# Performance work log

Hardware: AMD Instinct MI355X
Metric: run time of the kernel (lower is better)

The kernel has to match this reference:

```python
import jax, jax.numpy as jnp
import numpy as np

B, C, H, W = 2, 256, 48, 48
NH = 4          # heads (and SE ratio)
DK = C // NH    # 64


def conv1x1(x, w, b):
    # x: [B,Cin,H,W], w: [Cout,Cin], b: [Cout]
    return jnp.einsum('oc,bchw->bohw', w, x) + b[None, :, None, None]


def rtrans(q_in, k_in, v_in, qw, qb, kw, kb, vw, vb):
    b, c, h_, w_ = q_in.shape
    n = h_ * w_
    q = conv1x1(q_in, qw, qb).reshape(b, NH, DK, n).transpose(0, 1, 3, 2)  # [B,h,N,dk]
    k = conv1x1(k_in, kw, kb).reshape(b, NH, DK, n)                         # [B,h,dk,N]
    v = conv1x1(v_in, vw, vb).reshape(b, NH, DK, n)                         # [B,h,dk,N]
    scores = jnp.einsum('bhnd,bhdm->bhnm', q, k) / jnp.sqrt(jnp.asarray(DK, q.dtype))
    attn = jax.nn.softmax(scores, axis=-1)                                  # [B,h,N,N]
    out = jnp.einsum('bhdn,bhnm->bhdm', v, attn)                            # [B,h,dk,N]
    return out.reshape(b, c, h_, w_)


def setup_inputs() -> dict:
    key = jax.random.key(0)
    ks = jax.random.split(key, 16)
    s = 0.02
    d = {
        'x': jax.random.normal(ks[0], (B, C, H, W), jnp.float32),
        'y': jax.random.normal(ks[1], (B, C, H, W), jnp.float32),
        # RScaling: fc1 Conv2d(2C, C//ratio, 1), fc2 Conv2d(C//ratio, 2C, 1); ratio=NH
        'sc_fc1_w': jax.random.normal(ks[2], (C // NH, 2 * C), jnp.float32) * s,
        'sc_fc1_b': jnp.zeros((C // NH,), jnp.float32),
        'sc_fc2_w': jax.random.normal(ks[3], (2 * C, C // NH), jnp.float32) * s,
        'sc_fc2_b': jnp.zeros((2 * C,), jnp.float32),
        # RTrans 1
        't1_qw': jax.random.normal(ks[4], (C, C), jnp.float32) * s,
        't1_qb': jnp.zeros((C,), jnp.float32),
        't1_kw': jax.random.normal(ks[5], (C, C), jnp.float32) * s,
        't1_kb': jnp.zeros((C,), jnp.float32),
        't1_vw': jax.random.normal(ks[6], (C, C), jnp.float32) * s,
        't1_vb': jnp.zeros((C,), jnp.float32),
        # RTrans 2 (ST=True)
        't2_qw': jax.random.normal(ks[7], (C, C), jnp.float32) * s,
        't2_qb': jnp.zeros((C,), jnp.float32),
        't2_kw': jax.random.normal(ks[8], (C, C), jnp.float32) * s,
        't2_kb': jnp.zeros((C,), jnp.float32),
        't2_vw': jax.random.normal(ks[9], (C, C), jnp.float32) * s,
        't2_vb': jnp.zeros((C,), jnp.float32),
        # RGating: Conv2d(2C, 2, 1)
        'gate_w': jax.random.normal(ks[10], (2, 2 * C), jnp.float32) * s,
        'gate_b': jnp.zeros((2,), jnp.float32),
    }
    return d


def reference(x, y, sc_fc1_w, sc_fc1_b, sc_fc2_w, sc_fc2_b,
              t1_qw, t1_qb, t1_kw, t1_kb, t1_vw, t1_vb,
              t2_qw, t2_qb, t2_kw, t2_kb, t2_vw, t2_vb,
              gate_w, gate_b):
    c = x.shape[1]
    # --- RScaling (SE squeeze-excite on concatenated streams) ---
    cat = jnp.concatenate([x, y], axis=1)                       # [B,2C,H,W]
    pooled = cat.mean(axis=(2, 3), keepdims=True)               # [B,2C,1,1]
    f = conv1x1(jax.nn.relu(conv1x1(pooled, sc_fc1_w, sc_fc1_b)), sc_fc2_w, sc_fc2_b)
    g = jax.nn.sigmoid(f)                                       # [B,2C,1,1]
    x = x * g[:, :c] + x
    y = y * g[:, c:] + y
    # --- RTrans 1: x = attn(q=x, k=y, v=y) ---
    x = rtrans(x, y, y, t1_qw, t1_qb, t1_kw, t1_kb, t1_vw, t1_vb)
    # --- RTrans 2 (ST): y = attn(q=y, k=x_new, v=x_new) ---
    y = rtrans(y, x, x, t2_qw, t2_qb, t2_kw, t2_kb, t2_vw, t2_vb)
    # --- RGating ---
    gate = jax.nn.sigmoid(conv1x1(jnp.concatenate([x, y], axis=1), gate_w, gate_b))  # [B,2,H,W]
    x = x * gate[:, :1] + x
    y = y * gate[:, 1:] + y
    return (x, y)
```

## Files before the change

### kernel.cpp

```cpp
#include <hip/hip_runtime.h>
#include <hip/hip_bf16.h>
#include <math.h>

typedef __hip_bfloat16 bf16;
typedef unsigned short u16;
typedef __attribute__((ext_vector_type(8))) short short8;
typedef __attribute__((ext_vector_type(4))) float f32x4;

#define BB  2
#define CC  256
#define NHH 4
#define DKK 64
#define NN  2304
#define NT  36
#define NT2 18
#define MS  4
#define NTM 9
#define MFMA16(a,b,c) __builtin_amdgcn_mfma_f32_16x16x32_bf16(a, b, c, 0, 0, 0)

__device__ __forceinline__ float u2f(u16 u){ return __uint_as_float(((unsigned)u) << 16); }
__device__ __forceinline__ u16 f2u(float f){
    unsigned u = __float_as_uint(f);
    unsigned r = u + 0x7FFFu + ((u >> 16) & 1u);
    return (u16)(r >> 16);
}

__device__ __forceinline__ float ldv(const void* p, size_t i, int bf){
    return bf ? u2f(((const u16*)p)[i]) : ((const float*)p)[i];
}
__device__ __forceinline__ void stv(void* p, size_t i, float v, int bf){
    if (bf) ((u16*)p)[i] = f2u(v);
    else    ((float*)p)[i] = v;
}
__device__ __forceinline__ short8 ldw8(const void* p, size_t i, int bf){
    if (bf) return *(const short8*)((const u16*)p + i);
    const float* f = (const float*)p + i;
    short8 r;
    #pragma unroll
    for (int k = 0; k < 8; k++) r[k] = (short)f2u(f[k]);
    return r;
}

__global__ void detect_kernel(const void* __restrict__ x, int* __restrict__ flg){
    const u16* u = (const u16*)x;
    int t = threadIdx.x;
    bool ok = true;
    for (int i = 0; i < 8; i++){
        u16 v = u[t*8 + i];
        int e = (v >> 7) & 0xFF;
        ok = ok && (((v & 0x7FFF) == 0) || (e >= 96 && e <= 143));
    }
    unsigned long long b = __ballot(ok);
    if (t == 0) *flg = (b == 0xFFFFFFFFFFFFFFFFull) ? 1 : 0;
}

__global__ void pool_kernel(const void* __restrict__ x, const void* __restrict__ y,
                            const int* __restrict__ flg, float* __restrict__ pooled){
    int bf = *flg;
    int bid = blockIdx.x;
    int b = bid >> 9, cc = bid & 511;
    const void* src = (cc < CC) ? x : y;
    size_t base = ((size_t)b*CC + (cc & 255))*NN;
    float s = 0.f;
    for (int i = threadIdx.x; i < NN; i += 256) s += ldv(src, base + i, bf);
    __shared__ float red[4];
    for (int off = 32; off; off >>= 1) s += __shfl_down(s, off, 64);
    if ((threadIdx.x & 63) == 0) red[threadIdx.x >> 6] = s;
    __syncthreads();
    if (threadIdx.x == 0)
        pooled[bid] = (red[0]+red[1]+red[2]+red[3]) * (1.0f/(float)NN);
}

__global__ void se_fc1_kernel(const float* __restrict__ pooled,
                              const void* __restrict__ w1, const void* __restrict__ b1,
                              const int* __restrict__ flg, float* __restrict__ f1){
    int bf = *flg;
    int bid = blockIdx.x;
    int b = bid >> 6, f = bid & 63;
    int lane = threadIdx.x;
    const float* ps = pooled + b*512;
    float a = 0.f;
    #pragma unroll
    for (int k = 0; k < 8; k++){
        int c = lane*8 + k;
        a += ldv(w1, (size_t)f*512 + c, bf) * ps[c];
    }
    #pragma unroll
    for (int off = 32; off; off >>= 1) a += __shfl_down(a, off, 64);
    if (lane == 0)
        f1[b*64 + f] = fmaxf(a + ldv(b1, f, bf), 0.f);
}

__global__ void se_fc2_kernel(const float* __restrict__ f1,
                              const void* __restrict__ w2, const void* __restrict__ b2v,
                              const int* __restrict__ flg, float* __restrict__ gse){
    int bf = *flg;
    int b = blockIdx.x;
    int o = threadIdx.x;
    __shared__ float f1s[64];
    if (o < 64) f1s[o] = f1[b*64 + o];
    __syncthreads();
    float a = ldv(b2v, o, bf);
    #pragma unroll
    for (int j = 0; j < 64; j++) a += ldv(w2, (size_t)o*64 + j, bf) * f1s[j];
    gse[b*512 + o] = 1.f + 1.f/(1.f + __expf(-a));
}

__global__ void transpose2_kernel(const void* __restrict__ x, const void* __restrict__ y,
                                  const float* __restrict__ gse, const int* __restrict__ flg,
                                  u16* __restrict__ xsT, u16* __restrict__ ysT){
    int bf = *flg;
    int z = blockIdx.z;
    int b = z >> 1, which = z & 1;
    const void* src = which ? y : x;
    const float* gs = gse + b*512 + (which ? 256 : 0);
    u16* dst = which ? ysT : xsT;
    int ct = blockIdx.y, nt = blockIdx.x;
    int t = threadIdx.x;
    int nl = t & 63, cq = t >> 6;
    #pragma unroll
    for (int i = 0; i < 16; i++){
        int c = ct*64 + cq*16 + i;
        float v = ldv(src, ((size_t)b*CC + c)*NN + nt*64 + nl, bf) * gs[c];
        dst[((size_t)b*NN + nt*64 + nl)*CC + c] = f2u(v);
    }
}

__launch_bounds__(256)
__global__ void conv3_mfma(const u16* __restrict__ Xq, const u16* __restrict__ Xkv,
                           const void* __restrict__ wq, const void* __restrict__ bq,
                           const void* __restrict__ wk, const void* __restrict__ bk,
                           const void* __restrict__ wv, const void* __restrict__ bv_,
                           const int* __restrict__ flg,
                           u16* __restrict__ QT, u16* __restrict__ KT, u16* __restrict__ Vb){
    int bf = *flg;
    int z = blockIdx.z;
    int b = z / 3, op = z % 3;
    const u16* X = (op == 0) ? Xq : Xkv;
    const void* W    = (op == 0) ? wq : (op == 1) ? wk : wv;
    const void* bias = (op == 0) ? bq : (op == 1) ? bk : bv_;
    u16* Y = (op == 0) ? QT : (op == 1) ? KT : Vb;
    int transT = (op < 2);
    float oscale = (op == 1) ? 0.125f : 1.0f;
    int ot = blockIdx.y, nt = blockIdx.x;
    int lane = threadIdx.x & 63, wv_ = threadIdx.x >> 6;
    int c15 = lane & 15, quad = lane >> 4;
    const u16* Xb = X + ((size_t)b*NN + nt*64)*CC;
    int oa = ot*64 + wv_*16 + c15;
    f32x4 zf = {0.f,0.f,0.f,0.f};
    f32x4 acc[4] = {zf,zf,zf,zf};
    #pragma unroll
    for (int kc = 0; kc < CC; kc += 32){
        short8 aw = ldw8(W, (size_t)oa*CC + kc + quad*8, bf);
        #pragma unroll
        for (int j = 0; j < 4; j++){
            short8 bx = *(const short8*)(Xb + (size_t)(j*16 + c15)*CC + kc + quad*8);
            acc[j] = MFMA16(aw, bx, acc[j]);
        }
    }
    int od = ot*64 + wv_*16 + quad*4;
    float bvr[4];
    #pragma unroll
    for (int r = 0; r < 4; r++) bvr[r] = ldv(bias, od + r, bf);
    #pragma unroll
    for (int j = 0; j < 4; j++){
        int n = nt*64 + j*16 + c15;
        #pragma unroll
        for (int r = 0; r < 4; r++){
            int o = od + r;
            float val = (acc[j][r] + bvr[r]) * oscale;
            size_t idx = transT
              ? (((size_t)(b*NHH + (o >> 6))*NN + n)*DKK + (o & 63))
              : (((size_t)b*CC + o)*NN + n);
            Y[idx] = f2u(val);
        }
    }
}

__launch_bounds__(256)
__global__ void attn_stats_mfma(const u16* __restrict__ QT, const u16* __restrict__ KT,
                                float* __restrict__ gM, float* __restrict__ gL){
    int bh = blockIdx.y, ntile = blockIdx.x, ms = blockIdx.z;
    int lane = threadIdx.x & 63, wv = threadIdx.x >> 6;
    int c15 = lane & 15, quad = lane >> 4;
    const u16* Qb = QT + (size_t)bh*NN*DKK;
    const u16* Kb = KT + (size_t)bh*NN*DKK;
    size_t qo = (size_t)(ntile*64 + wv*16 + c15)*DKK + quad*8;
    short8 a0 = *(const short8*)(Qb + qo);
    short8 a1 = *(const short8*)(Qb + qo + 32);
    float ml[4] = {-3e38f,-3e38f,-3e38f,-3e38f};
    float ll[4] = {0.f,0.f,0.f,0.f};
    f32x4 z = {0.f,0.f,0.f,0.f};
    for (int it = 0; it < NTM; it++){
        int mt = ms*NTM + it;
        f32x4 s[4];
        #pragma unroll
        for (int j = 0; j < 4; j++){
            size_t ko = (size_t)(mt*64 + j*16 + c15)*DKK + quad*8;
            short8 b0 = *(const short8*)(Kb + ko);
            short8 b1 = *(const short8*)(Kb + ko + 32);
            f32x4 t = MFMA16(a0, b0, z);
            s[j]     = MFMA16(a1, b1, t);
        }
        #pragma unroll
        for (int r = 0; r < 4; r++){
            float v0 = s[0][r], v1 = s[1][r], v2 = s[2][r], v3 = s[3][r];
            float vmax = fmaxf(fmaxf(v0,v1), fmaxf(v2,v3));
            float mn = fmaxf(ml[r], vmax);
            float es = __expf(v0-mn)+__expf(v1-mn)+__expf(v2-mn)+__expf(v3-mn);
            ll[r] = ll[r]*__expf(ml[r]-mn) + es;
            ml[r] = mn;
        }
    }
    #pragma unroll
    for (int d = 1; d < 16; d <<= 1){
        #pragma unroll
        for (int r = 0; r < 4; r++){
            float mo = __shfl_xor(ml[r], d, 16);
            float lo = __shfl_xor(ll[r], d, 16);
            float mn = fmaxf(ml[r], mo);
            ll[r] = ll[r]*__expf(ml[r]-mn) + lo*__expf(mo-mn);
            ml[r] = mn;
        }
    }
    if (c15 == 0){
        #pragma unroll
        for (int r = 0; r < 4; r++){
            int n = ntile*64 + wv*16 + quad*4 + r;
            size_t o = ((size_t)ms*BB*NHH + bh)*NN + n;
            gM[o] = ml[r];
            gL[o] = ll[r];
        }
    }
}

__global__ void stats_combine(const float* __restrict__ gM, const float* __restrict__ gL,
                              float* __restrict__ M, float* __restrict__ Li){
    int idx = blockIdx.x*256 + threadIdx.x;
    if (idx >= BB*NHH*NN) return;
    float mm = -3e38f, ll = 0.f;
    #pragma unroll
    for (int ms = 0; ms < MS; ms++){
        float m = gM[(size_t)ms*BB*NHH*NN + idx];
        float l = gL[(size_t)ms*BB*NHH*NN + idx];
        float mn = fmaxf(mm, m);
        ll = ll*__expf(mm-mn) + l*__expf(m-mn);
        mm = mn;
    }
    M[idx]  = mm;
    Li[idx] = 1.f/ll;
}

__launch_bounds__(512)
__global__ void attn_out_mfma(const u16* __restrict__ QT, const u16* __restrict__ KT,
                              const u16* __restrict__ V, const float* __restrict__ M,
                              const float* __restrict__ Li, const int* __restrict__ flg,
                              void* __restrict__ O, size_t ooff, u16* __restrict__ OT){
    int bf = *flg;
    int bh = blockIdx.y, mtile = blockIdx.x;
    int tid = threadIdx.x;
    int lane = tid & 63, wv5 = tid >> 6;
    int g = wv5 >> 2, wv = wv5 & 3;
    int c15 = lane & 15, quad = lane >> 4;
    const u16* Qb = QT + (size_t)bh*NN*DKK;
    const u16* Kb = KT + (size_t)bh*NN*DKK;
    const u16* Vb = V + (size_t)bh*DKK*NN;
    const float* Mp = M + (size_t)bh*NN;
    const float* Lp = Li + (size_t)bh*NN;
    __shared__ __align__(16) u16 wT[2][2][64][72];
    __shared__ __align__(16) float osum[64][65];
    short8 kb0[4], kb1[4];
    #pragma unroll
    for (int j = 0; j < 4; j++){
        size_t ko = (size_t)(mtile*64 + j*16 + c15)*DKK + quad*8;
        kb0[j] = *(const short8*)(Kb + ko);
        kb1[j] = *(const short8*)(Kb + ko + 32);
    }
    f32x4 z = {0.f,0.f,0.f,0.f};
    f32x4 o4[4] = {z,z,z,z};
    for (int it = 0; it < NT2; it++){
        int nt = g*NT2 + it;
        int p = it & 1;
        size_t qo = (size_t)(nt*64 + wv*16 + c15)*DKK + quad*8;
        short8 a0 = *(const short8*)(Qb + qo);
        short8 a1 = *(const short8*)(Qb + qo + 32);
        f32x4 s[4];
        #pragma unroll
        for (int j = 0; j < 4; j++){
            f32x4 t = MFMA16(a0, kb0[j], z);
            s[j]    = MFMA16(a1, kb1[j], t);
        }
        int nb = nt*64 + wv*16 + quad*4;
        float Mr[4], iL[4];
        #pragma unroll
        for (int r = 0; r < 4; r++){ Mr[r] = Mp[nb+r]; iL[r] = Lp[nb+r]; }
        size_t vo = (size_t)(wv*16 + c15)*NN + nt*64 + quad*8;
        short8 av0 = *(const short8*)(Vb + vo);
        short8 av1 = *(const short8*)(Vb + vo + 32);
        #pragma unroll
        for (int j = 0; j < 4; j++){
            ushort4 pk;
            pk.x = f2u(__expf(s[j][0] - Mr[0]) * iL[0]);
            pk.y = f2u(__expf(s[j][1] - Mr[1]) * iL[1]);
            pk.z = f2u(__expf(s[j][2] - Mr[2]) * iL[2]);
            pk.w = f2u(__expf(s[j][3] - Mr[3]) * iL[3]);
            *(ushort4*)&wT[g][p][j*16 + c15][wv*16 + quad*4] = pk;
        }
        __syncthreads();
        #pragma unroll
        for (int j = 0; j < 4; j++){
            short8 b0 = *(const short8*)&wT[g][p][j*16 + c15][quad*8];
            short8 b1 = *(const short8*)&wT[g][p][j*16 + c15][32 + quad*8];
            o4[j] = MFMA16(av0, b0, o4[j]);
            o4[j] = MFMA16(av1, b1, o4[j]);
        }
    }
    if (g == 1){
        #pragma unroll
        for (int j = 0; j < 4; j++)
            #pragma unroll
            for (int r = 0; r < 4; r++)
                osum[wv*16 + quad*4 + r][j*16 + c15] = o4[j][r];
    }
    __syncthreads();
    if (g == 0){
        int brow = bh >> 2, head = bh & 3;
        #pragma unroll
        for (int j = 0; j < 4; j++){
            int m = mtile*64 + j*16 + c15;
            #pragma unroll
            for (int r = 0; r < 4; r++){
                int d = wv*16 + quad*4 + r;
                float val = o4[j][r] + osum[d][j*16 + c15];
                stv(O, ooff + ((size_t)brow*CC + head*DKK + d)*NN + m, val, bf);
                if (OT) OT[((size_t)brow*NN + m)*CC + head*DKK + d] = f2u(val);
            }
        }
    }
}

__global__ void gate_part_kernel(const void* __restrict__ out, const void* __restrict__ gw,
                                 const int* __restrict__ flg, float* __restrict__ gpart){
    int bf = *flg;
    const size_t SZ = (size_t)BB*CC*NN;
    int b = blockIdx.z, g = blockIdx.y;
    int nb = blockIdx.x*64;
    int t = threadIdx.x;
    int nl = t & 63, sub = t >> 6;
    __shared__ float r0[4][64], r1[4][64];
    float a0 = 0.f, a1 = 0.f;
    int cbase = g*128 + sub*32;
    for (int i = 0; i < 32; i++){
        int cc = cbase + i;
        size_t idx = (cc < 256 ? ((size_t)b*CC + cc)*NN
                               : SZ + ((size_t)b*CC + (cc-256))*NN) + nb + nl;
        float v = ldv(out, idx, bf);
        a0 += ldv(gw, cc, bf)*v;
        a1 += ldv(gw, 512 + cc, bf)*v;
    }
    r0[sub][nl] = a0; r1[sub][nl] = a1;
    __syncthreads();
    if (t < 64){
        float s0 = r0[0][t]+r0[1][t]+r0[2][t]+r0[3][t];
        float s1 = r1[0][t]+r1[1][t]+r1[2][t]+r1[3][t];
        int n = nb + t;
        gpart[(((size_t)b*4 + g)*2 + 0)*NN + n] = s0;
        gpart[(((size_t)b*4 + g)*2 + 1)*NN + n] = s1;
    }
}

__global__ void gate_combine_kernel(const float* __restrict__ gpart, const void* __restrict__ gb,
                                    const int* __restrict__ flg, float* __restrict__ gates){
    int bf = *flg;
    int idx = blockIdx.x*256 + threadIdx.x;
    if (idx >= BB*NN) return;
    int b = idx / NN, n = idx % NN;
    float s0 = ldv(gb, 0, bf), s1 = ldv(gb, 1, bf);
    #pragma unroll
    for (int g = 0; g < 4; g++){
        s0 += gpart[(((size_t)b*4 + g)*2 + 0)*NN + n];
        s1 += gpart[(((size_t)b*4 + g)*2 + 1)*NN + n];
    }
    gates[((size_t)b*2 + 0)*NN + n] = 1.f + 1.f/(1.f + __expf(-s0));
    gates[((size_t)b*2 + 1)*NN + n] = 1.f + 1.f/(1.f + __expf(-s1));
}

__global__ void rescale_kernel(const float* __restrict__ gates, const int* __restrict__ flg,
                               void* __restrict__ out){
    int bf = *flg;
    const size_t SZ = (size_t)BB*CC*NN;
    const size_t nq = (2*SZ) >> 2;
    for (size_t u = (size_t)blockIdx.x*256 + threadIdx.x; u < nq; u += (size_t)gridDim.x*256){
        size_t flat = u*4;
        int half = (int)(flat / SZ);
        size_t rem = flat % SZ;
        int b = (int)(rem / ((size_t)CC*NN));
        int n = (int)(rem % NN);
        const float* gp = gates + ((size_t)b*2 + half)*NN + n;
        #pragma unroll
        for (int k = 0; k < 4; k++)
            stv(out, flat + k, ldv(out, flat + k, bf) * gp[k], bf);
    }
}

extern "C" void kernel_launch(void* const* d_in, const int* in_sizes, int n_in,
                              void* d_out, int out_size, void* d_ws, size_t ws_size,
                              hipStream_t stream){
    (void)in_sizes; (void)n_in; (void)out_size; (void)ws_size;
    const void* x    = d_in[0];
    const void* y    = d_in[1];
    const void* sc1w = d_in[2];
    const void* sc1b = d_in[3];
    const void* sc2w = d_in[4];
    const void* sc2b = d_in[5];
    const void *t1qw = d_in[6],  *t1qb = d_in[7];
    const void *t1kw = d_in[8],  *t1kb = d_in[9];
    const void *t1vw = d_in[10], *t1vb = d_in[11];
    const void *t2qw = d_in[12], *t2qb = d_in[13];
    const void *t2kw = d_in[14], *t2kb = d_in[15];
    const void *t2vw = d_in[16], *t2vb = d_in[17];
    const void *gw   = d_in[18], *gb   = d_in[19];

    const size_t SZ = (size_t)BB*CC*NN;
    const size_t BHN = (size_t)BB*NHH*NN;
    char* wsb = (char*)d_ws;
    int*   flg    = (int*)wsb;
    float* pooled = (float*)(wsb + 16);
    float* f1     = pooled + 1024;
    float* gse    = f1 + 128;
    float* Mb     = gse + 1024;
    float* Lb     = Mb + BHN;
    float* gM     = Lb + BHN;
    float* gL     = gM + MS*BHN;
    float* gpart  = gL + MS*BHN;
    float* gates  = gpart + (size_t)BB*4*2*NN;
    u16* xsT = (u16*)(gates + (size_t)BB*2*NN);
    u16* ysT = xsT + SZ;
    u16* QT  = ysT + SZ;
    u16* KT  = QT + SZ;
    u16* Vb  = KT + SZ;

    dim3 tg2(NT, 4, BB*2);
    dim3 cg3(NT, 4, BB*3);
    dim3 sg(NT, BB*NHH, MS);
    dim3 ag(NT, BB*NHH);
    dim3 gg(NT, 4, BB);

    detect_kernel<<<1, 64, 0, stream>>>(x, flg);
    pool_kernel<<<1024, 256, 0, stream>>>(x, y, flg, pooled);
    se_fc1_kernel<<<BB*64, 64, 0, stream>>>(pooled, sc1w, sc1b, flg, f1);
    se_fc2_kernel<<<BB, 512, 0, stream>>>(f1, sc2w, sc2b, flg, gse);

    transpose2_kernel<<<tg2, 256, 0, stream>>>(x, y, gse, flg, xsT, ysT);

    conv3_mfma<<<cg3, 256, 0, stream>>>(xsT, ysT, t1qw, t1qb, t1kw, t1kb, t1vw, t1vb,
                                        flg, QT, KT, Vb);
    attn_stats_mfma<<<sg, 256, 0, stream>>>(QT, KT, gM, gL);
    stats_combine<<<72, 256, 0, stream>>>(gM, gL, Mb, Lb);
    attn_out_mfma<<<ag, 512, 0, stream>>>(QT, KT, Vb, Mb, Lb, flg, d_out, 0, xsT);

    conv3_mfma<<<cg3, 256, 0, stream>>>(ysT, xsT, t2qw, t2qb, t2kw, t2kb, t2vw, t2vb,
                                        flg, QT, KT, Vb);
    attn_stats_mfma<<<sg, 256, 0, stream>>>(QT, KT, gM, gL);
    stats_combine<<<72, 256, 0, stream>>>(gM, gL, Mb, Lb);
    attn_out_mfma<<<ag, 512, 0, stream>>>(QT, KT, Vb, Mb, Lb, flg, d_out, SZ, (u16*)nullptr);

    gate_part_kernel<<<gg, 256, 0, stream>>>(d_out, gw, flg, gpart);
    gate_combine_kernel<<<18, 256, 0, stream>>>(gpart, gb, flg, gates);
    rescale_kernel<<<1024, 256, 0, stream>>>(gates, flg, d_out);
}
```

Measured before the change: 407.7 us.

## Split attention output over key chunks with atomic accumulation and finalize pass

The attention-output kernel now splits the N reduction across four grid slices (blockIdx.z) of 256-thread blocks instead of two in-block wave groups. Each slice accumulates its partial output into a zeroed fp32 buffer with atomicAdd, and a new finalize kernel writes the result and the transposed bf16 copy. Q and V tiles are also prefetched one iteration ahead. The aim is more blocks and better occupancy for the 72-block grid, at the cost of atomic traffic, an extra zeroing pass inside stats_combine, and one more kernel launch per attention.

Result: slower. 429.3 us (+5.3%).

```diff
diff --git a/kernel.cpp b/kernel.cpp
--- a/kernel.cpp
+++ b/kernel.cpp
@@ -13,7 +13,6 @@
 #define DKK 64
 #define NN  2304
 #define NT  36
-#define NT2 18
 #define MS  4
 #define NTM 9
 #define MFMA16(a,b,c) __builtin_amdgcn_mfma_f32_16x16x32_bf16(a, b, c, 0, 0, 0)
@@ -235,40 +234,41 @@
 }
 
 __global__ void stats_combine(const float* __restrict__ gM, const float* __restrict__ gL,
-                              float* __restrict__ M, float* __restrict__ Li){
+                              float* __restrict__ M, float* __restrict__ Li,
+                              float* __restrict__ Obuf){
     int idx = blockIdx.x*256 + threadIdx.x;
-    if (idx >= BB*NHH*NN) return;
-    float mm = -3e38f, ll = 0.f;
-    #pragma unroll
-    for (int ms = 0; ms < MS; ms++){
-        float m = gM[(size_t)ms*BB*NHH*NN + idx];
-        float l = gL[(size_t)ms*BB*NHH*NN + idx];
-        float mn = fmaxf(mm, m);
-        ll = ll*__expf(mm-mn) + l*__expf(m-mn);
-        mm = mn;
-    }
-    M[idx]  = mm;
-    Li[idx] = 1.f/ll;
-}
-
-__launch_bounds__(512)
+    if (idx < BB*NHH*NN){
+        float mm = -3e38f, ll = 0.f;
+        #pragma unroll
+        for (int ms = 0; ms < MS; ms++){
+            float m = gM[(size_t)ms*BB*NHH*NN + idx];
+            float l = gL[(size_t)ms*BB*NHH*NN + idx];
+            float mn = fmaxf(mm, m);
+            ll = ll*__expf(mm-mn) + l*__expf(m-mn);
+            mm = mn;
+        }
+        M[idx]  = mm;
+        Li[idx] = 1.f/ll;
+    }
+    const size_t nq = ((size_t)BB*CC*NN) >> 2;
+    float4 z4 = make_float4(0.f, 0.f, 0.f, 0.f);
+    for (size_t u = idx; u < nq; u += (size_t)18432)
+        ((float4*)Obuf)[u] = z4;
+}
+
+__launch_bounds__(256)
 __global__ void attn_out_mfma(const u16* __restrict__ QT, const u16* __restrict__ KT,
                               const u16* __restrict__ V, const float* __restrict__ M,
-                              const float* __restrict__ Li, const int* __restrict__ flg,
-                              void* __restrict__ O, size_t ooff, u16* __restrict__ OT){
-    int bf = *flg;
-    int bh = blockIdx.y, mtile = blockIdx.x;
-    int tid = threadIdx.x;
-    int lane = tid & 63, wv5 = tid >> 6;
-    int g = wv5 >> 2, wv = wv5 & 3;
+                              const float* __restrict__ Li, float* __restrict__ Obuf){
+    int bh = blockIdx.y, mtile = blockIdx.x, ms = blockIdx.z;
+    int lane = threadIdx.x & 63, wv = threadIdx.x >> 6;
     int c15 = lane & 15, quad = lane >> 4;
     const u16* Qb = QT + (size_t)bh*NN*DKK;
     const u16* Kb = KT + (size_t)bh*NN*DKK;
     const u16* Vb = V + (size_t)bh*DKK*NN;
     const float* Mp = M + (size_t)bh*NN;
     const float* Lp = Li + (size_t)bh*NN;
-    __shared__ __align__(16) u16 wT[2][2][64][72];
-    __shared__ __align__(16) float osum[64][65];
+    __shared__ __align__(16) u16 wT[2][64][72];
     short8 kb0[4], kb1[4];
     #pragma unroll
     for (int j = 0; j < 4; j++){
@@ -278,25 +278,35 @@
     }
     f32x4 z = {0.f,0.f,0.f,0.f};
     f32x4 o4[4] = {z,z,z,z};
-    for (int it = 0; it < NT2; it++){
-        int nt = g*NT2 + it;
+    int nt0 = ms*NTM;
+    size_t qo = (size_t)(nt0*64 + wv*16 + c15)*DKK + quad*8;
+    short8 a0 = *(const short8*)(Qb + qo);
+    short8 a1 = *(const short8*)(Qb + qo + 32);
+    size_t vo = (size_t)(wv*16 + c15)*NN + nt0*64 + quad*8;
+    short8 av0 = *(const short8*)(Vb + vo);
+    short8 av1 = *(const short8*)(Vb + vo + 32);
+    for (int it = 0; it < NTM; it++){
+        int nt = ms*NTM + it;
         int p = it & 1;
-        size_t qo = (size_t)(nt*64 + wv*16 + c15)*DKK + quad*8;
-        short8 a0 = *(const short8*)(Qb + qo);
-        short8 a1 = *(const short8*)(Qb + qo + 32);
         f32x4 s[4];
         #pragma unroll
         for (int j = 0; j < 4; j++){
             f32x4 t = MFMA16(a0, kb0[j], z);
             s[j]    = MFMA16(a1, kb1[j], t);
         }
+        short8 a0n = a0, a1n = a1, av0n = av0, av1n = av1;
+        if (it + 1 < NTM){
+            size_t qn = (size_t)((nt+1)*64 + wv*16 + c15)*DKK + quad*8;
+            a0n = *(const short8*)(Qb + qn);
+            a1n = *(const short8*)(Qb + qn + 32);
+            size_t vn = (size_t)(wv*16 + c15)*NN + (nt+1)*64 + quad*8;
+            av0n = *(const short8*)(Vb + vn);
+            av1n = *(const short8*)(Vb + vn + 32);
+        }
         int nb = nt*64 + wv*16 + quad*4;
         float Mr[4], iL[4];
         #pragma unroll
         for (int r = 0; r < 4; r++){ Mr[r] = Mp[nb+r]; iL[r] = Lp[nb+r]; }
-        size_t vo = (size_t)(wv*16 + c15)*NN + nt*64 + quad*8;
-        short8 av0 = *(const short8*)(Vb + vo);
-        short8 av1 = *(const short8*)(Vb + vo + 32);
         #pragma unroll
         for (int j = 0; j < 4; j++){
             ushort4 pk;
@@ -304,37 +314,50 @@
             pk.y = f2u(__expf(s[j][1] - Mr[1]) * iL[1]);
             pk.z = f2u(__expf(s[j][2] - Mr[2]) * iL[2]);
             pk.w = f2u(__expf(s[j][3] - Mr[3]) * iL[3]);
-            *(ushort4*)&wT[g][p][j*16 + c15][wv*16 + quad*4] = pk;
+            *(ushort4*)&wT[p][j*16 + c15][wv*16 + quad*4] = pk;
         }
         __syncthreads();
         #pragma unroll
         for (int j = 0; j < 4; j++){
-            short8 b0 = *(const short8*)&wT[g][p][j*16 + c15][quad*8];
-            short8 b1 = *(const short8*)&wT[g][p][j*16 + c15][32 + quad*8];
+            short8 b0 = *(const short8*)&wT[p][j*16 + c15][quad*8];
+            short8 b1 = *(const short8*)&wT[p][j*16 + c15][32 + quad*8];
             o4[j] = MFMA16(av0, b0, o4[j]);
             o4[j] = MFMA16(av1, b1, o4[j]);
         }
-    }
-    if (g == 1){
-        #pragma unroll
-        for (int j = 0; j < 4; j++)
-            #pragma unroll
-            for (int r = 0; r < 4; r++)
-                osum[wv*16 + quad*4 + r][j*16 + c15] = o4[j][r];
-    }
-    __syncthreads();
-    if (g == 0){
-        int brow = bh >> 2, head = bh & 3;
-        #pragma unroll
-        for (int j = 0; j < 4; j++){
-            int m = mtile*64 + j*16 + c15;
-            #pragma unroll
-            for (int r = 0; r < 4; r++){
-                int d = wv*16 + quad*4 + r;
-                float val = o4[j][r] + osum[d][j*16 + c15];
-                stv(O, ooff + ((size_t)brow*CC + head*DKK + d)*NN + m, val, bf);
-                if (OT) OT[((size_t)brow*NN + m)*CC + head*DKK + d] = f2u(val);
-            }
+        a0 = a0n; a1 = a1n; av0 = av0n; av1 = av1n;
+    }
+    #pragma unroll
+    for (int j = 0; j < 4; j++){
+        int m = mtile*64 + j*16 + c15;
+        #pragma unroll
+        for (int r = 0; r < 4; r++){
+            int d = wv*16 + quad*4 + r;
+            atomicAdd(&Obuf[((size_t)bh*DKK + d)*NN + m], o4[j][r]);
+        }
+    }
+}
+
+__global__ void attn_finalize(const float* __restrict__ Obuf, const int* __restrict__ flg,
+                              void* __restrict__ O, size_t ooff, u16* __restrict__ OT){
+    int bf = *flg;
+    int b = blockIdx.z, ct = blockIdx.y, mt = blockIdx.x;
+    int bh = b*NHH + ct;
+    int t = threadIdx.x;
+    int il = t & 63, grp = t >> 6;
+    __shared__ u16 lds[64][66];
+    #pragma unroll
+    for (int i = 0; i < 16; i++){
+        int d = grp*16 + i;
+        float v = Obuf[((size_t)bh*DKK + d)*NN + mt*64 + il];
+        stv(O, ooff + ((size_t)b*CC + ct*64 + d)*NN + mt*64 + il, v, bf);
+        if (OT) lds[il][d] = f2u(v);
+    }
+    if (OT){
+        __syncthreads();
+        #pragma unroll
+        for (int i = 0; i < 16; i++){
+            int m = grp*16 + i;
+            OT[((size_t)b*NN + mt*64 + m)*CC + ct*64 + il] = lds[m][il];
         }
     }
 }
@@ -434,7 +457,8 @@
     float* gL     = gM + MS*BHN;
     float* gpart  = gL + MS*BHN;
     float* gates  = gpart + (size_t)BB*4*2*NN;
-    u16* xsT = (u16*)(gates + (size_t)BB*2*NN);
+    float* Obuf   = gates + (size_t)BB*2*NN;
+    u16* xsT = (u16*)(Obuf + SZ);
     u16* ysT = xsT + SZ;
     u16* QT  = ysT + SZ;
     u16* KT  = QT + SZ;
@@ -443,7 +467,8 @@
     dim3 tg2(NT, 4, BB*2);
     dim3 cg3(NT, 4, BB*3);
     dim3 sg(NT, BB*NHH, MS);
-    dim3 ag(NT, BB*NHH);
+    dim3 ag(NT, BB*NHH, MS);
+    dim3 fg(NT, 4, BB);
     dim3 gg(NT, 4, BB);
 
     detect_kernel<<<1, 64, 0, stream>>>(x, flg);
@@ -456,14 +481,16 @@
     conv3_mfma<<<cg3, 256, 0, stream>>>(xsT, ysT, t1qw, t1qb, t1kw, t1kb, t1vw, t1vb,
                                         flg, QT, KT, Vb);
     attn_stats_mfma<<<sg, 256, 0, stream>>>(QT, KT, gM, gL);
-    stats_combine<<<72, 256, 0, stream>>>(gM, gL, Mb, Lb);
-    attn_out_mfma<<<ag, 512, 0, stream>>>(QT, KT, Vb, Mb, Lb, flg, d_out, 0, xsT);
+    stats_combine<<<72, 256, 0, stream>>>(gM, gL, Mb, Lb, Obuf);
+    attn_out_mfma<<<ag, 256, 0, stream>>>(QT, KT, Vb, Mb, Lb, Obuf);
+    attn_finalize<<<fg, 256, 0, stream>>>(Obuf, flg, d_out, 0, xsT);
 
     conv3_mfma<<<cg3, 256, 0, stream>>>(ysT, xsT, t2qw, t2qb, t2kw, t2kb, t2vw, t2vb,
                                         flg, QT, KT, Vb);
     attn_stats_mfma<<<sg, 256, 0, stream>>>(QT, KT, gM, gL);
-    stats_combine<<<72, 256, 0, stream>>>(gM, gL, Mb, Lb);
-    attn_out_mfma<<<ag, 512, 0, stream>>>(QT, KT, Vb, Mb, Lb, flg, d_out, SZ, (u16*)nullptr);
+    stats_combine<<<72, 256, 0, stream>>>(gM, gL, Mb, Lb, Obuf);
+    attn_out_mfma<<<ag, 256, 0, stream>>>(QT, KT, Vb, Mb, Lb, Obuf);
+    attn_finalize<<<fg, 256, 0, stream>>>(Obuf, flg, d_out, SZ, (u16*)nullptr);
 
     gate_part_kernel<<<gg, 256, 0, stream>>>(d_out, gw, flg, gpart);
     gate_combine_kernel<<<18, 256, 0, stream>>>(gpart, gb, flg, gates);
```
